# Kernel tuning notes

Measured on AMD Instinct MI355X. Metric: run time of the kernel, lower is better.

## Reference

```python
import jax, jax.numpy as jnp
import numpy as np

D_MODEL = 256
N_LAYERS = 4
D_STATE = 16
EXPAND = 2
D_CONV = 4
D_INNER = EXPAND * D_MODEL
DT_RANK = (D_MODEL + 15) // 16  # ceil(d_model/16) = 16
BATCH = 8
SEQ = 2048
EPS = 1e-5


def setup_inputs() -> dict:
    key = jax.random.key(0)
    ks = jax.random.split(key, 12)
    rn = lambda k, s, sc=0.02: jax.random.normal(k, s, dtype=jnp.float32) * sc
    A_log = jnp.log(jnp.broadcast_to(jnp.arange(1, D_STATE + 1, dtype=jnp.float32),
                                     (N_LAYERS, D_INNER, D_STATE)))
    return {
        "x": jax.random.normal(ks[0], (BATCH, SEQ, 2), dtype=jnp.float32),
        "w_in": rn(ks[1], (D_MODEL, 2), 0.5),
        "b_in": jnp.zeros((D_MODEL,), jnp.float32),
        "norm_w": jnp.ones((N_LAYERS, D_MODEL), jnp.float32),
        "in_proj_w": rn(ks[2], (N_LAYERS, 2 * D_INNER, D_MODEL)),
        "conv_w": rn(ks[3], (N_LAYERS, D_INNER, 1, D_CONV), 0.1),
        "conv_b": jnp.zeros((N_LAYERS, D_INNER), jnp.float32),
        "x_proj_w": rn(ks[4], (N_LAYERS, DT_RANK + 2 * D_STATE, D_INNER)),
        "dt_proj_w": rn(ks[5], (N_LAYERS, D_INNER, DT_RANK), 0.1),
        "dt_proj_b": rn(ks[6], (N_LAYERS, D_INNER), 0.1),
        "A_log": A_log,
        "D_skip": jnp.ones((N_LAYERS, D_INNER), jnp.float32),
        "out_proj_w": rn(ks[7], (N_LAYERS, D_MODEL, D_INNER)),
        "w_head": rn(ks[8], (1, D_MODEL), 0.1),
        "b_head": jnp.zeros((1,), jnp.float32),
    }


def _rmsnorm(x, w):
    return x * jax.lax.rsqrt(jnp.mean(x * x, axis=-1, keepdims=True) + EPS) * w


def _causal_dw_conv(x, w, b):
    # x: (B, L, C); w: (C, 1, K) depthwise; causal left-pad K-1
    xt = jnp.swapaxes(x, 1, 2)  # (B, C, L)
    y = jax.lax.conv_general_dilated(xt, w, (1,), [(D_CONV - 1, 0)],
                                     dimension_numbers=("NCH", "OIH", "NCH"),
                                     feature_group_count=D_INNER)
    return jnp.swapaxes(y + b[None, :, None], 1, 2)


def _selective_scan(u, delta, A, Bm, Cm, Dp):
    # u, delta: (B, L, E); A: (E, N); Bm, Cm: (B, L, N); Dp: (E,)
    dA = jnp.exp(delta[..., None] * A)                 # (B, L, E, N)
    dBu = (delta * u)[..., None] * Bm[:, :, None, :]   # (B, L, E, N)

    def step(h, t):
        dA_t, dBu_t = t
        h = dA_t * h + dBu_t
        return h, h

    h0 = jnp.zeros((u.shape[0], A.shape[0], A.shape[1]), u.dtype)
    _, hs = jax.lax.scan(step, h0, (jnp.swapaxes(dA, 0, 1), jnp.swapaxes(dBu, 0, 1)))
    y = jnp.einsum("lben,bln->ble", hs, Cm)            # (B, L, E)
    return y + u * Dp


def _mamba_block(x, in_w, cw, cb, xp_w, dtw, dtb, A_log, Dp, out_w):
    xz = x @ in_w.T                                    # (B, L, 2E)
    u, z = jnp.split(xz, 2, axis=-1)
    u = jax.nn.silu(_causal_dw_conv(u, cw, cb))
    dbc = u @ xp_w.T                                   # (B, L, dt_rank + 2N)
    delta = jax.nn.softplus(dbc[..., :DT_RANK] @ dtw.T + dtb)
    Bm = dbc[..., DT_RANK:DT_RANK + D_STATE]
    Cm = dbc[..., DT_RANK + D_STATE:]
    y = _selective_scan(u, delta, -jnp.exp(A_log), Bm, Cm, Dp)
    return (y * jax.nn.silu(z)) @ out_w.T


def reference(x, w_in, b_in, norm_w, in_proj_w, conv_w, conv_b, x_proj_w,
              dt_proj_w, dt_proj_b, A_log, D_skip, out_proj_w, w_head, b_head):
    h = x @ w_in.T + b_in                              # (B, L, d_model)
    for i in range(N_LAYERS):
        h = h + _mamba_block(_rmsnorm(h, norm_w[i]), in_proj_w[i], conv_w[i],
                             conv_b[i], x_proj_w[i], dt_proj_w[i], dt_proj_b[i],
                             A_log[i], D_skip[i], out_proj_w[i])
    return (h @ w_head.T + b_head)[..., 0]             # (B, L)
```

## Files before the change

kernel.cpp:

```cpp
#include <hip/hip_runtime.h>
#include <hip/hip_bf16.h>

#define BATCH 8
#define SEQ   2048
#define DM    256
#define DI    512
#define DS    16
#define DTR   16
#define NL    4
#define ROWS  (BATCH*SEQ)
#define NCH   32
#define CHL   64
#define NF    576

typedef __attribute__((ext_vector_type(8))) __bf16 bh8;
typedef __attribute__((ext_vector_type(4))) float f4;

#if __has_builtin(__builtin_amdgcn_exp2f)
#define EXP2(x) __builtin_amdgcn_exp2f(x)
#else
#define EXP2(x) exp2f(x)
#endif
#define LOG2E 1.4426950408889634f

__device__ __forceinline__ float bf2f(unsigned short u) {
    union { unsigned int i; float f; } v; v.i = ((unsigned int)u) << 16; return v.f;
}
__device__ __forceinline__ float4 us4f(ushort4 q) {
    return make_float4(bf2f(q.x), bf2f(q.y), bf2f(q.z), bf2f(q.w));
}
__device__ __forceinline__ float ldg1(const void* p, int i, int bf) {
    if (bf) return bf2f(((const unsigned short*)p)[i]);
    return ((const float*)p)[i];
}
__device__ __forceinline__ float4 ldg4(const void* p, int i, int bf) {
    if (bf) return us4f(*(const ushort4*)(((const unsigned short*)p) + i));
    return *(const float4*)(((const float*)p) + i);
}
__device__ __forceinline__ unsigned short f2bs(float f) {
    union { float f; unsigned u; } x; x.f = f;
    unsigned r = (x.u + 0x7fffu + ((x.u >> 16) & 1u)) >> 16;
    return (unsigned short)r;
}
__device__ __forceinline__ float fsilu(float x) {
    return x * __builtin_amdgcn_rcpf(1.0f + __expf(-x));
}
__device__ __forceinline__ float fsoftplus(float x) {
    return (x > 15.0f) ? x : __logf(1.0f + __expf(x));
}
__device__ __forceinline__ void pow16(float e1, float* pw) {
    float p2 = e1 * e1, p3 = p2 * e1, p4 = p2 * p2;
    float p5 = p4 * e1, p6 = p4 * p2, p7 = p4 * p3, p8 = p4 * p4;
    pw[0] = e1; pw[1] = p2; pw[2] = p3; pw[3] = p4;
    pw[4] = p5; pw[5] = p6; pw[6] = p7; pw[7] = p8;
    pw[8]  = p8 * e1; pw[9]  = p8 * p2; pw[10] = p8 * p3; pw[11] = p8 * p4;
    pw[12] = p8 * p5; pw[13] = p8 * p6; pw[14] = p8 * p7; pw[15] = p8 * p8;
}

typedef const __attribute__((address_space(1))) unsigned int* gas_t;
typedef __attribute__((address_space(3))) unsigned int* las_t;
__device__ __forceinline__ void gl16(const void* g, void* l) {
    __builtin_amdgcn_global_load_lds((gas_t)g, (las_t)l, 16, 0, 0);
}

__global__ void k_probe(const void* x, const void* A_log, int* flag) {
    int t = threadIdx.x;
    float v = bf2f(((const unsigned short*)x)[2 * t]);
    int bad = (fabsf(v) < 32.0f) ? 0 : 1;
    for (int o = 1; o < 64; o <<= 1) bad += __shfl_xor(bad, o);
    int bf = (bad > 8) ? 0 : 1;
    int nb = 0;
    for (int j = 0; j < 64; j++) {
        int e = ((j * 64 + t) * 17) & 32767;
        int n = e & 15;
        float a = ldg1(A_log, e, bf);
        float ea = __expf(a);
        if (fabsf(ea - (float)(n + 1)) > 0.02f * (float)(n + 1)) nb = 1;
    }
    for (int o = 1; o < 64; o <<= 1) nb += __shfl_xor(nb, o);
    if (t == 0) { flag[0] = bf; flag[1] = (nb == 0) ? 1 : 0; }
}

__global__ __launch_bounds__(256) void k_prep(const void* dtw, const void* xpw,
                                              const void* ipw, const void* norm_w,
                                              unsigned short* Wc, unsigned short* Wip,
                                              const int* flag) {
    int bf = *flag;
    int blk = blockIdx.x;
    int t = threadIdx.x;
    if (blk < NL * NF) {
        int l = blk / NF, r = blk % NF;
        unsigned short* out = Wc + ((size_t)l * NF + r) * DI;
#pragma unroll
        for (int p = 0; p < 2; p++) {
            int k = t + p * 256;
            float v = 0.0f;
            if (r < 512) {
                const int db = l * DI * DTR + r * DTR;
                const int xb = l * 48 * DI;
#pragma unroll
                for (int j = 0; j < 16; j++)
                    v = fmaf(ldg1(dtw, db + j, bf), ldg1(xpw, xb + j * DI + k, bf), v);
            } else if (r < 544) {
                v = ldg1(xpw, l * 48 * DI + (16 + r - 512) * DI + k, bf);
            }
            out[k] = f2bs(v);
        }
    } else {
        int b2 = blk - NL * NF;
        int l = b2 >> 10, r = b2 & 1023;
        float v = ldg1(ipw, (l * 1024 + r) * 256 + t, bf) * ldg1(norm_w, l * 256 + t, bf);
        Wip[((size_t)l * 1024 + r) * 256 + t] = f2bs(v);
    }
}

__global__ __launch_bounds__(256) void k_inproj(const void* x, const void* w_in, const void* b_in,
                                                unsigned short* h, float* rssq, const int* flag) {
    int bf = *flag;
    int row = blockIdx.x, e = threadIdx.x;
    float x0 = ldg1(x, row * 2 + 0, bf), x1 = ldg1(x, row * 2 + 1, bf);
    float w0 = ldg1(w_in, e * 2 + 0, bf), w1 = ldg1(w_in, e * 2 + 1, bf);
    float bb = ldg1(b_in, e, bf);
    unsigned short hb = f2bs(fmaf(x0, w0, fmaf(x1, w1, bb)));
    h[(size_t)row * DM + e] = hb;
    float hv = bf2f(hb);
    float ss = hv * hv;
#pragma unroll
    for (int o = 1; o < 64; o <<= 1) ss += __shfl_xor(ss, o);
    if ((e & 63) == 0) rssq[(size_t)row * 4 + (e >> 6)] = ss;
}

#define ASTR 72

__global__ __launch_bounds__(256, 4) void k_ipconv(const unsigned short* A, const unsigned short* W,
                                                   int w_off, unsigned short* xz, unsigned short* u,
                                                   const float* rssq, const void* cw, const void* cb,
                                                   int layer, const int* flag) {
    int bf = *flag;
    constexpr int K = DM;
    constexpr int TSTR = 136;
    __shared__ unsigned short SMEM[144 * TSTR];
    unsigned short* As  = SMEM;
    unsigned short* As2 = SMEM + 8192;
    unsigned short* Ws  = SMEM + 9216;

    int bm = blockIdx.x, bn = blockIdx.y;
    bool ublk = (bn < 4);
    int t = threadIdx.x;
    int w = t >> 6, lane = t & 63;
    int wm = w >> 1, wn = w & 1;
    int lr = lane & 15, quad = lane >> 4;
    int crow = lane >> 3;
    int ccol = ((lane & 7) ^ (lane >> 3)) * 8;

    f4 acc[4][4];
    f4 acc5[4];
#pragma unroll
    for (int i = 0; i < 4; i++) {
        acc5[i] = f4{0.f, 0.f, 0.f, 0.f};
#pragma unroll
        for (int j = 0; j < 4; j++) acc[i][j] = f4{0.f, 0.f, 0.f, 0.f};
    }

    for (int k0 = 0; k0 < K; k0 += 64) {
        __syncthreads();
#pragma unroll
        for (int i = 0; i < 4; i++) {
            int ci = w * 4 + i;
            int r = ci * 8 + crow;
            gl16(A + (size_t)(bm * 128 + r) * K + k0 + ccol, &As[ci * 512]);
        }
        if (ublk && w < 2) {
            int rg = bm * 128 - 16 + w * 8 + crow;
            if (rg < 0) rg = 0;
            gl16(A + (size_t)rg * K + k0 + ccol, &As2[w * 512]);
        }
#pragma unroll
        for (int i = 0; i < 4; i++) {
            int ci = w * 4 + i;
            int r = ci * 8 + crow;
            gl16(W + (size_t)w_off + (size_t)(bn * 128 + r) * K + k0 + ccol, &Ws[ci * 512]);
        }
        __syncthreads();
#pragma unroll
        for (int ks = 0; ks < 64; ks += 32) {
            int csw = (ks + quad * 8) ^ ((lr & 7) << 3);
            bh8 af[4];
#pragma unroll
            for (int i = 0; i < 4; i++)
                af[i] = *(const bh8*)&As[(wm * 64 + i * 16 + lr) * 64 + csw];
            bh8 wf[4];
#pragma unroll
            for (int j = 0; j < 4; j++)
                wf[j] = *(const bh8*)&Ws[(wn * 64 + j * 16 + lr) * 64 + csw];
#pragma unroll
            for (int i = 0; i < 4; i++)
#pragma unroll
                for (int j = 0; j < 4; j++)
                    acc[i][j] = __builtin_amdgcn_mfma_f32_16x16x32_bf16(af[i], wf[j], acc[i][j], 0, 0, 0);
            if (ublk && wm == 0) {
                bh8 a5 = *(const bh8*)&As2[lr * 64 + csw];
#pragma unroll
                for (int j = 0; j < 4; j++)
                    acc5[j] = __builtin_amdgcn_mfma_f32_16x16x32_bf16(a5, wf[j], acc5[j], 0, 0, 0);
            }
        }
    }
    __syncthreads();
    unsigned short* Tile = SMEM;
#pragma unroll
    for (int i = 0; i < 4; i++) {
        int rl = wm * 64 + i * 16 + quad * 4;
        float sc4[4];
#pragma unroll
        for (int r = 0; r < 4; r++) {
            float4 q4 = *(const float4*)&rssq[(size_t)(bm * 128 + rl + r) * 4];
            sc4[r] = rsqrtf((q4.x + q4.y + q4.z + q4.w) * (1.0f / (float)DM) + 1e-5f);
        }
#pragma unroll
        for (int j = 0; j < 4; j++) {
            int cl = wn * 64 + j * 16 + lr;
#pragma unroll
            for (int r = 0; r < 4; r++)
                Tile[(rl + r) * TSTR + cl] = f2bs(acc[i][j][r] * sc4[r]);
        }
    }
    if (ublk && wm == 0) {
#pragma unroll
        for (int r = 0; r < 4; r++) {
            int er = quad * 4 + r;
            int rg = bm * 128 - 16 + er;
            if (rg < 0) rg = 0;
            float4 q4 = *(const float4*)&rssq[(size_t)rg * 4];
            float sc = rsqrtf((q4.x + q4.y + q4.z + q4.w) * (1.0f / (float)DM) + 1e-5f);
#pragma unroll
            for (int j = 0; j < 4; j++) {
                int cl = wn * 64 + j * 16 + lr;
                Tile[(128 + er) * TSTR + cl] = f2bs(acc5[j][r] * sc);
            }
        }
    }
    __syncthreads();
    if (!ublk) {
#pragma unroll
        for (int i = 0; i < 8; i++) {
            int ch = t + i * 256;
            int r = ch >> 4, qc = (ch & 15) * 8;
            uint4 v = *(uint4*)&Tile[r * TSTR + qc];
            *(uint4*)&xz[(size_t)(bm * 128 + r) * 1024 + bn * 128 + qc] = v;
        }
    } else {
        int col4 = t & 31, rowg = t >> 5;
        int c0 = col4 * 4;
        int dg = bn * 128 + c0;
        float4 wv0 = ldg4(cw, (layer * DI + dg + 0) * 4, bf);
        float4 wv1 = ldg4(cw, (layer * DI + dg + 1) * 4, bf);
        float4 wv2 = ldg4(cw, (layer * DI + dg + 2) * 4, bf);
        float4 wv3 = ldg4(cw, (layer * DI + dg + 3) * 4, bf);
        float4 bb = ldg4(cb, layer * DI + dg, bf);
        bool bstart = ((bm & 15) == 0);
        int r0 = rowg * 16;
        auto ldrow = [&](int q) -> float4 {
            if (q < 0) {
                if (bstart) return make_float4(0.f, 0.f, 0.f, 0.f);
                return us4f(*(const ushort4*)&Tile[(144 + q) * TSTR + c0]);
            }
            return us4f(*(const ushort4*)&Tile[q * TSTR + c0]);
        };
        float4 xm3 = ldrow(r0 - 3), xm2 = ldrow(r0 - 2), xm1 = ldrow(r0 - 1);
        for (int rr = r0; rr < r0 + 16; rr++) {
            float4 x0 = us4f(*(const ushort4*)&Tile[rr * TSTR + c0]);
            float a0 = bb.x; a0 = fmaf(wv0.x, xm3.x, a0); a0 = fmaf(wv0.y, xm2.x, a0); a0 = fmaf(wv0.z, xm1.x, a0); a0 = fmaf(wv0.w, x0.x, a0);
            float a1 = bb.y; a1 = fmaf(wv1.x, xm3.y, a1); a1 = fmaf(wv1.y, xm2.y, a1); a1 = fmaf(wv1.z, xm1.y, a1); a1 = fmaf(wv1.w, x0.y, a1);
            float a2 = bb.z; a2 = fmaf(wv2.x, xm3.z, a2); a2 = fmaf(wv2.y, xm2.z, a2); a2 = fmaf(wv2.z, xm1.z, a2); a2 = fmaf(wv2.w, x0.z, a2);
            float a3 = bb.w; a3 = fmaf(wv3.x, xm3.w, a3); a3 = fmaf(wv3.y, xm2.w, a3); a3 = fmaf(wv3.z, xm1.w, a3); a3 = fmaf(wv3.w, x0.w, a3);
            ushort4 o = { f2bs(fsilu(a0)), f2bs(fsilu(a1)), f2bs(fsilu(a2)), f2bs(fsilu(a3)) };
            *(ushort4*)&u[(size_t)(bm * 128 + rr) * DI + dg] = o;
            xm3 = xm2; xm2 = xm1; xm1 = x0;
        }
    }
}

template <int BN, bool ADD, bool SCALE, bool RSUM, bool WINT>
__global__ __launch_bounds__(256, 4) void k_mfma(const unsigned short* A, const void* W, int w_off,
                                                 unsigned short* Cp, float* rssq,
                                                 int N, int K, const int* flag) {
    int bf = *flag;
    __shared__ unsigned short SMEM[(128 + BN) * ASTR];
    unsigned short* As = SMEM;
    unsigned short* Ws = SMEM + 128 * 64;
    constexpr int NT = BN / 32;
    constexpr int TSTR = BN + 8;

    int bm = blockIdx.x, bn = blockIdx.y;
    int t = threadIdx.x;
    int w = t >> 6, lane = t & 63;
    int wm = w >> 1, wn = w & 1;
    int lr = lane & 15, quad = lane >> 4;
    int crow = lane >> 3;
    int ccol = ((lane & 7) ^ (lane >> 3)) * 8;

    f4 acc[4][NT];
#pragma unroll
    for (int i = 0; i < 4; i++)
#pragma unroll
        for (int j = 0; j < NT; j++) acc[i][j] = f4{0.f, 0.f, 0.f, 0.f};

    for (int k0 = 0; k0 < K; k0 += 64) {
        __syncthreads();
#pragma unroll
        for (int i = 0; i < 4; i++) {
            int ci = w * 4 + i;
            int r = ci * 8 + crow;
            gl16(A + (size_t)(bm * 128 + r) * K + k0 + ccol, &As[ci * 512]);
        }
        if (WINT || bf) {
#pragma unroll
            for (int i = 0; i < BN / 32; i++) {
                int ci = w * (BN / 32) + i;
                int r = ci * 8 + crow;
                gl16((const unsigned short*)W + (size_t)w_off +
                         (size_t)(bn * BN + r) * K + k0 + ccol,
                     &Ws[ci * 512]);
            }
        } else {
#pragma unroll
            for (int i = 0; i < BN * 8 / 256; i++) {
                int ch = t + i * 256;
                int r = ch >> 3, kc = (ch & 7) * 8;
                size_t off = (size_t)w_off + (size_t)(bn * BN + r) * K + k0 + kc;
                const float* src = (const float*)W + off;
                float4 a0 = *(const float4*)src;
                float4 a1 = *(const float4*)(src + 4);
                ushort4 v0 = { f2bs(a0.x), f2bs(a0.y), f2bs(a0.z), f2bs(a0.w) };
                ushort4 v1 = { f2bs(a1.x), f2bs(a1.y), f2bs(a1.z), f2bs(a1.w) };
                unsigned short* dst = &Ws[r * 64 + (kc ^ ((r & 7) << 3))];
                *(ushort4*)dst = v0;
                *(ushort4*)(dst + 4) = v1;
            }
        }
        __syncthreads();
#pragma unroll
        for (int ks = 0; ks < 64; ks += 32) {
            int csw = (ks + quad * 8) ^ ((lr & 7) << 3);
            bh8 af[4];
#pragma unroll
            for (int i = 0; i < 4; i++)
                af[i] = *(const bh8*)&As[(wm * 64 + i * 16 + lr) * 64 + csw];
            bh8 wf[NT];
#pragma unroll
            for (int j = 0; j < NT; j++)
                wf[j] = *(const bh8*)&Ws[(wn * (BN / 2) + j * 16 + lr) * 64 + csw];
#pragma unroll
            for (int i = 0; i < 4; i++)
#pragma unroll
                for (int j = 0; j < NT; j++)
                    acc[i][j] = __builtin_amdgcn_mfma_f32_16x16x32_bf16(af[i], wf[j], acc[i][j], 0, 0, 0);
        }
    }
    __syncthreads();
    unsigned short* Tile = SMEM;
#pragma unroll
    for (int i = 0; i < 4; i++) {
        int rl = wm * 64 + i * 16 + quad * 4;
        float sc4[4];
        if (SCALE) {
#pragma unroll
            for (int r = 0; r < 4; r++) {
                float4 q4 = *(const float4*)&rssq[(size_t)(bm * 128 + rl + r) * 4];
                sc4[r] = rsqrtf((q4.x + q4.y + q4.z + q4.w) * (1.0f / (float)DM) + 1e-5f);
            }
        }
#pragma unroll
        for (int j = 0; j < NT; j++) {
            int cl = wn * (BN / 2) + j * 16 + lr;
#pragma unroll
            for (int r = 0; r < 4; r++) {
                float vv = acc[i][j][r];
                if (SCALE) vv *= sc4[r];
                Tile[(rl + r) * TSTR + cl] = f2bs(vv);
            }
        }
    }
    __syncthreads();
    constexpr int CPT = 128 * BN / 8 / 256;
#pragma unroll
    for (int i = 0; i < CPT; i++) {
        int ch = t + i * 256;
        int r = ch / (BN / 8), qc = (ch % (BN / 8)) * 8;
        uint4 v = *(uint4*)&Tile[r * TSTR + qc];
        size_t gidx = (size_t)(bm * 128 + r) * N + bn * BN + qc;
        if (ADD) {
            uint4 c = *(uint4*)&Cp[gidx];
            unsigned short* vp = (unsigned short*)&v;
            unsigned short* cp2 = (unsigned short*)&c;
            uint4 ov;
            unsigned short* op = (unsigned short*)&ov;
            float ssq = 0.0f;
#pragma unroll
            for (int e = 0; e < 8; e++) {
                op[e] = f2bs(bf2f(vp[e]) + bf2f(cp2[e]));
                if (RSUM) { float hv = bf2f(op[e]); ssq = fmaf(hv, hv, ssq); }
            }
            *(uint4*)&Cp[gidx] = ov;
            if (RSUM) {
#pragma unroll
                for (int o2 = 1; o2 < 8; o2 <<= 1) ssq += __shfl_xor(ssq, o2);
                if ((lane & 7) == 0) rssq[(size_t)(bm * 128 + r) * 4 + bn] = ssq;
            }
        } else {
            *(uint4*)&Cp[gidx] = v;
        }
    }
}

__global__ __launch_bounds__(256, 4) void k_fused(const unsigned short* A, const unsigned short* Wc,
                                                  int w_off, unsigned short* delta, float* BC,
                                                  const void* dtb, int layer, const int* flag) {
    int bf = *flag;
    __shared__ unsigned short SMEM[(128 + 64) * ASTR];
    unsigned short* As = SMEM;
    unsigned short* Ws = SMEM + 128 * 64;
    constexpr int TSTR = 72;

    int bm = blockIdx.x, bn = blockIdx.y;
    int t = threadIdx.x;
    int w = t >> 6, lane = t & 63;
    int wm = w >> 1, wn = w & 1;
    int lr = lane & 15, quad = lane >> 4;
    int crow = lane >> 3;
    int ccol = ((lane & 7) ^ (lane >> 3)) * 8;

    f4 acc[4][2];
#pragma unroll
    for (int i = 0; i < 4; i++)
#pragma unroll
        for (int j = 0; j < 2; j++) acc[i][j] = f4{0.f, 0.f, 0.f, 0.f};

    for (int k0 = 0; k0 < DI; k0 += 64) {
        __syncthreads();
#pragma unroll
        for (int i = 0; i < 4; i++) {
            int ci = w * 4 + i;
            int r = ci * 8 + crow;
            gl16(A + (size_t)(bm * 128 + r) * DI + k0 + ccol, &As[ci * 512]);
        }
#pragma unroll
        for (int i = 0; i < 2; i++) {
            int ci = w * 2 + i;
            int r = ci * 8 + crow;
            gl16(Wc + (size_t)w_off + (size_t)(bn * 64 + r) * DI + k0 + ccol, &Ws[ci * 512]);
        }
        __syncthreads();
#pragma unroll
        for (int ks = 0; ks < 64; ks += 32) {
            int csw = (ks + quad * 8) ^ ((lr & 7) << 3);
            bh8 af[4];
#pragma unroll
            for (int i = 0; i < 4; i++)
                af[i] = *(const bh8*)&As[(wm * 64 + i * 16 + lr) * 64 + csw];
            bh8 wf[2];
#pragma unroll
            for (int j = 0; j < 2; j++)
                wf[j] = *(const bh8*)&Ws[(wn * 32 + j * 16 + lr) * 64 + csw];
#pragma unroll
            for (int i = 0; i < 4; i++)
#pragma unroll
                for (int j = 0; j < 2; j++)
                    acc[i][j] = __builtin_amdgcn_mfma_f32_16x16x32_bf16(af[i], wf[j], acc[i][j], 0, 0, 0);
        }
    }
    if (bn < 8) {
        __syncthreads();
        unsigned short* Tile = SMEM;
#pragma unroll
        for (int i = 0; i < 4; i++) {
            int rl = wm * 64 + i * 16 + quad * 4;
#pragma unroll
            for (int j = 0; j < 2; j++) {
                int cl = wn * 32 + j * 16 + lr;
                float bb = ldg1(dtb, layer * DI + bn * 64 + cl, bf);
#pragma unroll
                for (int r = 0; r < 4; r++)
                    Tile[(rl + r) * TSTR + cl] = f2bs(fsoftplus(acc[i][j][r] + bb));
            }
        }
        __syncthreads();
#pragma unroll
        for (int i = 0; i < 4; i++) {
            int ch = t + i * 256;
            int r = ch >> 3, qc = (ch & 7) * 8;
            uint4 v = *(uint4*)&Tile[r * TSTR + qc];
            *(uint4*)&delta[(size_t)(bm * 128 + r) * DI + bn * 64 + qc] = v;
        }
    } else {
#pragma unroll
        for (int i = 0; i < 4; i++) {
            int row0 = bm * 128 + wm * 64 + i * 16 + quad * 4;
#pragma unroll
            for (int j = 0; j < 2; j++) {
                int col = bn * 64 + wn * 32 + j * 16 + lr;
                if (col < 544) {
#pragma unroll
                    for (int r = 0; r < 4; r++)
                        BC[(size_t)(row0 + r) * 32 + (col - 512)] = acc[i][j][r];
                }
            }
        }
    }
}

__global__ __launch_bounds__(256) void k_scan1(const unsigned short* delta, const unsigned short* u,
                                               const float* BC, const void* A_log, float* Sb, float* E,
                                               int layer, const int* flag) {
    int bf = flag[0], sA = flag[1];
    int x = blockIdx.x;
    int dg = x & 1, c = (x >> 1) & (NCH - 1), b = x >> 6;
    int tid = threadIdx.x;
    int d = dg * 256 + tid;
    int t0 = c * CHL;

    __shared__ float sB[CHL][16];
    {
        int r = tid >> 2, q = tid & 3;
        *(float4*)&sB[r][q * 4] =
            *(const float4*)(BC + ((size_t)b * SEQ + t0 + r) * 32 + q * 4);
    }

    float A2[16];
#pragma unroll
    for (int n4 = 0; n4 < 4; n4++) {
        float4 a4 = ldg4(A_log, (layer * DI + d) * DS + n4 * 4, bf);
        A2[n4 * 4 + 0] = -__expf(a4.x) * LOG2E;
        A2[n4 * 4 + 1] = -__expf(a4.y) * LOG2E;
        A2[n4 * 4 + 2] = -__expf(a4.z) * LOG2E;
        A2[n4 * 4 + 3] = -__expf(a4.w) * LOG2E;
    }
    float h[16];
#pragma unroll
    for (int n = 0; n < 16; n++) h[n] = 0.0f;
    float S = 0.0f;

    const unsigned short* dp = delta + ((size_t)b * SEQ + t0) * DI + d;
    const unsigned short* up = u + ((size_t)b * SEQ + t0) * DI + d;

    float dl0[4], uu0[4];
#pragma unroll
    for (int j = 0; j < 4; j++) { dl0[j] = bf2f(dp[j * DI]); uu0[j] = bf2f(up[j * DI]); }
    __syncthreads();

    for (int s = 0; s < CHL / 4; s++) {
        int sn = (s + 1 < CHL / 4) ? (s + 1) : s;
        float dl1[4], uu1[4];
#pragma unroll
        for (int j = 0; j < 4; j++) {
            dl1[j] = bf2f(dp[(sn * 4 + j) * DI]);
            uu1[j] = bf2f(up[(sn * 4 + j) * DI]);
        }
#pragma unroll
        for (int j = 0; j < 4; j++) {
            int t = s * 4 + j;
            float dlt = dl0[j], uu = uu0[j];
            float du = dlt * uu;
            S += dlt;
            if (sA) {
                float pw[16];
                pow16(EXP2(-dlt * LOG2E), pw);
#pragma unroll
                for (int n4 = 0; n4 < 4; n4++) {
                    float4 Bv = *(const float4*)&sB[t][n4 * 4];
                    int n = n4 * 4;
                    h[n + 0] = fmaf(pw[n + 0], h[n + 0], du * Bv.x);
                    h[n + 1] = fmaf(pw[n + 1], h[n + 1], du * Bv.y);
                    h[n + 2] = fmaf(pw[n + 2], h[n + 2], du * Bv.z);
                    h[n + 3] = fmaf(pw[n + 3], h[n + 3], du * Bv.w);
                }
            } else {
#pragma unroll
                for (int n4 = 0; n4 < 4; n4++) {
                    float4 Bv = *(const float4*)&sB[t][n4 * 4];
                    int n = n4 * 4;
                    float a0 = EXP2(dlt * A2[n + 0]); h[n + 0] = fmaf(a0, h[n + 0], du * Bv.x);
                    float a1 = EXP2(dlt * A2[n + 1]); h[n + 1] = fmaf(a1, h[n + 1], du * Bv.y);
                    float a2 = EXP2(dlt * A2[n + 2]); h[n + 2] = fmaf(a2, h[n + 2], du * Bv.z);
                    float a3 = EXP2(dlt * A2[n + 3]); h[n + 3] = fmaf(a3, h[n + 3], du * Bv.w);
                }
            }
        }
#pragma unroll
        for (int j = 0; j < 4; j++) { dl0[j] = dl1[j]; uu0[j] = uu1[j]; }
    }
    Sb[((size_t)b * NCH + c) * DI + d] = S;
    float* Ed = E + (((size_t)b * NCH + c) * DI + d) * DS;
#pragma unroll
    for (int n4 = 0; n4 < 4; n4++)
        *(float4*)(Ed + n4 * 4) = make_float4(h[n4 * 4], h[n4 * 4 + 1], h[n4 * 4 + 2], h[n4 * 4 + 3]);
}

__global__ __launch_bounds__(256) void k_stitch(const float* Sb, const void* A_log, float* E,
                                                int layer, const int* flag) {
    int bf = flag[0];
    int g = blockIdx.x * 256 + threadIdx.x;
    int b = g >> 13, r = g & 8191;
    int d = r >> 4;
    float A2a = -__expf(ldg1(A_log, (layer * DI + d) * DS + (r & 15), bf)) * LOG2E;
    size_t ebase = (size_t)b * NCH * (DI * DS) + r;
    float H = 0.0f;
    for (int c = 0; c < NCH; c++) {
        float p = EXP2(A2a * Sb[((size_t)b * NCH + c) * DI + d]);
        size_t idx = ebase + (size_t)c * (DI * DS);
        float e = E[idx];
        E[idx] = H;
        H = fmaf(p, H, e);
    }
}

__global__ __launch_bounds__(256) void k_scan2(const unsigned short* delta, const unsigned short* u,
                                               const float* BC, const void* A_log, const void* D_skip,
                                               const unsigned short* xz, const float* E,
                                               unsigned short* g, int layer, const int* flag) {
    int bf = flag[0], sA = flag[1];
    int x = blockIdx.x;
    int dg = x & 1, c = (x >> 1) & (NCH - 1), b = x >> 6;
    int tid = threadIdx.x;
    int d = dg * 256 + tid;
    int t0 = c * CHL;

    __shared__ float sBC[CHL][32];
#pragma unroll
    for (int k2 = 0; k2 < 2; k2++) {
        int fi = k2 * 256 + tid;
        int r = fi >> 3, q = fi & 7;
        *(float4*)&sBC[r][q * 4] =
            *(const float4*)(BC + ((size_t)b * SEQ + t0 + r) * 32 + q * 4);
    }

    float A2[16];
#pragma unroll
    for (int n4 = 0; n4 < 4; n4++) {
        float4 a4 = ldg4(A_log, (layer * DI + d) * DS + n4 * 4, bf);
        A2[n4 * 4 + 0] = -__expf(a4.x) * LOG2E;
        A2[n4 * 4 + 1] = -__expf(a4.y) * LOG2E;
        A2[n4 * 4 + 2] = -__expf(a4.z) * LOG2E;
        A2[n4 * 4 + 3] = -__expf(a4.w) * LOG2E;
    }
    float Dp = ldg1(D_skip, layer * DI + d, bf);

    float h[16];
    const float* E0 = E + (((size_t)b * NCH + c) * DI + d) * DS;
#pragma unroll
    for (int n4 = 0; n4 < 4; n4++) {
        float4 h4 = *(const float4*)(E0 + n4 * 4);
        h[n4 * 4 + 0] = h4.x; h[n4 * 4 + 1] = h4.y; h[n4 * 4 + 2] = h4.z; h[n4 * 4 + 3] = h4.w;
    }

    const unsigned short* dp = delta + ((size_t)b * SEQ + t0) * DI + d;
    const unsigned short* up = u + ((size_t)b * SEQ + t0) * DI + d;
    const unsigned short* zp = xz + ((size_t)b * SEQ + t0) * (2 * DI) + DI + d;
    unsigned short* gp = g + ((size_t)b * SEQ + t0) * DI + d;

    float dl0[4], uu0[4], zz0[4];
#pragma unroll
    for (int j = 0; j < 4; j++) {
        dl0[j] = bf2f(dp[j * DI]); uu0[j] = bf2f(up[j * DI]); zz0[j] = bf2f(zp[j * (2 * DI)]);
    }
    __syncthreads();

    for (int s = 0; s < CHL / 4; s++) {
        int sn = (s + 1 < CHL / 4) ? (s + 1) : s;
        float dl1[4], uu1[4], zz1[4];
#pragma unroll
        for (int j = 0; j < 4; j++) {
            dl1[j] = bf2f(dp[(sn * 4 + j) * DI]);
            uu1[j] = bf2f(up[(sn * 4 + j) * DI]);
            zz1[j] = bf2f(zp[(sn * 4 + j) * (2 * DI)]);
        }
#pragma unroll
        for (int j = 0; j < 4; j++) {
            int t = s * 4 + j;
            float dlt = dl0[j], uu = uu0[j], zz = zz0[j];
            float du = dlt * uu;
            float y = 0.0f;
            if (sA) {
                float pw[16];
                pow16(EXP2(-dlt * LOG2E), pw);
#pragma unroll
                for (int n4 = 0; n4 < 4; n4++) {
                    float4 Bv = *(const float4*)&sBC[t][n4 * 4];
                    float4 Cv = *(const float4*)&sBC[t][16 + n4 * 4];
                    int n = n4 * 4;
                    h[n + 0] = fmaf(pw[n + 0], h[n + 0], du * Bv.x); y = fmaf(Cv.x, h[n + 0], y);
                    h[n + 1] = fmaf(pw[n + 1], h[n + 1], du * Bv.y); y = fmaf(Cv.y, h[n + 1], y);
                    h[n + 2] = fmaf(pw[n + 2], h[n + 2], du * Bv.z); y = fmaf(Cv.z, h[n + 2], y);
                    h[n + 3] = fmaf(pw[n + 3], h[n + 3], du * Bv.w); y = fmaf(Cv.w, h[n + 3], y);
                }
            } else {
#pragma unroll
                for (int n4 = 0; n4 < 4; n4++) {
                    float4 Bv = *(const float4*)&sBC[t][n4 * 4];
                    float4 Cv = *(const float4*)&sBC[t][16 + n4 * 4];
                    int n = n4 * 4;
                    float a0 = EXP2(dlt * A2[n + 0]); h[n + 0] = fmaf(a0, h[n + 0], du * Bv.x); y = fmaf(Cv.x, h[n + 0], y);
                    float a1 = EXP2(dlt * A2[n + 1]); h[n + 1] = fmaf(a1, h[n + 1], du * Bv.y); y = fmaf(Cv.y, h[n + 1], y);
                    float a2 = EXP2(dlt * A2[n + 2]); h[n + 2] = fmaf(a2, h[n + 2], du * Bv.z); y = fmaf(Cv.z, h[n + 2], y);
                    float a3 = EXP2(dlt * A2[n + 3]); h[n + 3] = fmaf(a3, h[n + 3], du * Bv.w); y = fmaf(Cv.w, h[n + 3], y);
                }
            }
            float yt = fmaf(uu, Dp, y);
            gp[(size_t)t * DI] = f2bs(yt * fsilu(zz));
        }
#pragma unroll
        for (int j = 0; j < 4; j++) { dl0[j] = dl1[j]; uu0[j] = uu1[j]; zz0[j] = zz1[j]; }
    }
}

__global__ __launch_bounds__(256) void k_head(const unsigned short* h, const void* w_head,
                                              const void* b_head, void* out, const int* flag) {
    int bf = *flag;
    int wv = threadIdx.x >> 6, ln = threadIdx.x & 63;
    int row = blockIdx.x * 4 + wv;
    float4 v = us4f(*(const ushort4*)(h + (size_t)row * DM + ln * 4));
    float4 w = ldg4(w_head, ln * 4, bf);
    float s = v.x * w.x + v.y * w.y + v.z * w.z + v.w * w.w;
    for (int o = 1; o < 64; o <<= 1) s += __shfl_xor(s, o);
    if (ln == 0) {
        s += ldg1(b_head, 0, bf);
        if (bf) ((__hip_bfloat16*)out)[row] = __float2bfloat16(s);
        else    ((float*)out)[row] = s;
    }
}

extern "C" void kernel_launch(void* const* d_in, const int* in_sizes, int n_in,
                              void* d_out, int out_size, void* d_ws, size_t ws_size,
                              hipStream_t stream) {
    (void)in_sizes; (void)n_in; (void)out_size; (void)ws_size;
    const void* x      = d_in[0];
    const void* w_in   = d_in[1];
    const void* b_in   = d_in[2];
    const void* norm_w = d_in[3];
    const void* ipw    = d_in[4];
    const void* cw     = d_in[5];
    const void* cb     = d_in[6];
    const void* xpw    = d_in[7];
    const void* dtw    = d_in[8];
    const void* dtb    = d_in[9];
    const void* A_log  = d_in[10];
    const void* D_skip = d_in[11];
    const void* opw    = d_in[12];
    const void* w_head = d_in[13];
    const void* b_head = d_in[14];

    float* ws    = (float*)d_ws;
    unsigned short* h     = (unsigned short*)ws;
    float*          rssq  = ws + 4194304;
    float*          Sb    = ws + 4194304;
    float*          E     = ws + 4718592;
    unsigned short* xz    = (unsigned short*)(ws + 8388608);
    unsigned short* u     = (unsigned short*)(ws + 25165824);
    float*          BC    = ws + 33554432;
    unsigned short* delta = (unsigned short*)(ws + 34340864);
    unsigned short* Wcomb = (unsigned short*)(ws + 38535168);
    unsigned short* Wipc  = (unsigned short*)(ws + 39124992);
    int*            flag  = (int*)(ws + 42729472);

    k_probe<<<1, 64, 0, stream>>>(x, A_log, flag);
    k_prep<<<NL * NF + NL * 1024, 256, 0, stream>>>(dtw, xpw, ipw, norm_w, Wcomb, Wipc, flag);
    k_inproj<<<ROWS, 256, 0, stream>>>(x, w_in, b_in, h, rssq, flag);

    for (int layer = 0; layer < NL; layer++) {
        k_ipconv<<<dim3(ROWS / 128, 8), 256, 0, stream>>>(
            h, Wipc, layer * 2 * DI * DM, xz, u, rssq, cw, cb, layer, flag);
        k_fused<<<dim3(ROWS / 128, NF / 64), 256, 0, stream>>>(
            u, Wcomb, layer * NF * DI, delta, BC, dtb, layer, flag);
        k_scan1<<<BATCH * NCH * 2, 256, 0, stream>>>(delta, u, BC, A_log, Sb, E, layer, flag);
        k_stitch<<<BATCH * DI * DS / 256, 256, 0, stream>>>(Sb, A_log, E, layer, flag);
        k_scan2<<<BATCH * NCH * 2, 256, 0, stream>>>(delta, u, BC, A_log, D_skip, xz, E,
                                                     u , layer, flag);
        k_mfma<64, true, false, true, false><<<dim3(ROWS / 128, DM / 64), 256, 0, stream>>>(
            u, opw, layer * DM * DI, h, rssq, DM, DI, flag);
    }

    k_head<<<ROWS / 4, 256, 0, stream>>>(h, w_head, b_head, d_out, flag);
}
```

Measured before the change: 578.4 us.

## Split scan state dimension across two half-waves to double scan parallelism

The chunked scan kernels now assign each channel to two lanes, each holding 8 of the 16 state elements, and launch twice as many blocks. The partial C·h outputs are combined with a cross-half-wave shuffle, and only one lane writes each output. This is meant to raise occupancy and latency hiding in the scan, which previously had only 512 blocks with 16-element register state per thread. The cost is that both lanes redundantly load delta, u and z, compute pow16 or exp, and pay an extra shuffle per timestep, and the global loads are less coalesced (32 channels per wave instead of 64).

```diff
diff --git a/kernel.cpp b/kernel.cpp
--- a/kernel.cpp
+++ b/kernel.cpp
@@ -515,9 +515,11 @@
                                                int layer, const int* flag) {
     int bf = flag[0], sA = flag[1];
     int x = blockIdx.x;
-    int dg = x & 1, c = (x >> 1) & (NCH - 1), b = x >> 6;
+    int dg = x & 3, c = (x >> 2) & (NCH - 1), b = x >> 7;
     int tid = threadIdx.x;
-    int d = dg * 256 + tid;
+    int wv = tid >> 6, lane = tid & 63;
+    int ch = lane & 31, sh = lane >> 5;
+    int d = dg * 128 + wv * 32 + ch;
     int t0 = c * CHL;
 
     __shared__ float sB[CHL][16];
@@ -527,18 +529,18 @@
             *(const float4*)(BC + ((size_t)b * SEQ + t0 + r) * 32 + q * 4);
     }
 
-    float A2[16];
-#pragma unroll
-    for (int n4 = 0; n4 < 4; n4++) {
-        float4 a4 = ldg4(A_log, (layer * DI + d) * DS + n4 * 4, bf);
+    float A2[8];
+#pragma unroll
+    for (int n4 = 0; n4 < 2; n4++) {
+        float4 a4 = ldg4(A_log, (layer * DI + d) * DS + sh * 8 + n4 * 4, bf);
         A2[n4 * 4 + 0] = -__expf(a4.x) * LOG2E;
         A2[n4 * 4 + 1] = -__expf(a4.y) * LOG2E;
         A2[n4 * 4 + 2] = -__expf(a4.z) * LOG2E;
         A2[n4 * 4 + 3] = -__expf(a4.w) * LOG2E;
     }
-    float h[16];
-#pragma unroll
-    for (int n = 0; n < 16; n++) h[n] = 0.0f;
+    float h[8];
+#pragma unroll
+    for (int n = 0; n < 8; n++) h[n] = 0.0f;
     float S = 0.0f;
 
     const unsigned short* dp = delta + ((size_t)b * SEQ + t0) * DI + d;
@@ -567,18 +569,18 @@
                 float pw[16];
                 pow16(EXP2(-dlt * LOG2E), pw);
 #pragma unroll
-                for (int n4 = 0; n4 < 4; n4++) {
-                    float4 Bv = *(const float4*)&sB[t][n4 * 4];
+                for (int n4 = 0; n4 < 2; n4++) {
+                    float4 Bv = *(const float4*)&sB[t][sh * 8 + n4 * 4];
                     int n = n4 * 4;
-                    h[n + 0] = fmaf(pw[n + 0], h[n + 0], du * Bv.x);
-                    h[n + 1] = fmaf(pw[n + 1], h[n + 1], du * Bv.y);
-                    h[n + 2] = fmaf(pw[n + 2], h[n + 2], du * Bv.z);
-                    h[n + 3] = fmaf(pw[n + 3], h[n + 3], du * Bv.w);
+                    h[n + 0] = fmaf(pw[sh * 8 + n + 0], h[n + 0], du * Bv.x);
+                    h[n + 1] = fmaf(pw[sh * 8 + n + 1], h[n + 1], du * Bv.y);
+                    h[n + 2] = fmaf(pw[sh * 8 + n + 2], h[n + 2], du * Bv.z);
+                    h[n + 3] = fmaf(pw[sh * 8 + n + 3], h[n + 3], du * Bv.w);
                 }
             } else {
 #pragma unroll
-                for (int n4 = 0; n4 < 4; n4++) {
-                    float4 Bv = *(const float4*)&sB[t][n4 * 4];
+                for (int n4 = 0; n4 < 2; n4++) {
+                    float4 Bv = *(const float4*)&sB[t][sh * 8 + n4 * 4];
                     int n = n4 * 4;
                     float a0 = EXP2(dlt * A2[n + 0]); h[n + 0] = fmaf(a0, h[n + 0], du * Bv.x);
                     float a1 = EXP2(dlt * A2[n + 1]); h[n + 1] = fmaf(a1, h[n + 1], du * Bv.y);
@@ -590,10 +592,10 @@
 #pragma unroll
         for (int j = 0; j < 4; j++) { dl0[j] = dl1[j]; uu0[j] = uu1[j]; }
     }
-    Sb[((size_t)b * NCH + c) * DI + d] = S;
-    float* Ed = E + (((size_t)b * NCH + c) * DI + d) * DS;
-#pragma unroll
-    for (int n4 = 0; n4 < 4; n4++)
+    if (sh == 0) Sb[((size_t)b * NCH + c) * DI + d] = S;
+    float* Ed = E + (((size_t)b * NCH + c) * DI + d) * DS + sh * 8;
+#pragma unroll
+    for (int n4 = 0; n4 < 2; n4++)
         *(float4*)(Ed + n4 * 4) = make_float4(h[n4 * 4], h[n4 * 4 + 1], h[n4 * 4 + 2], h[n4 * 4 + 3]);
 }
 
@@ -621,9 +623,11 @@
                                                unsigned short* g, int layer, const int* flag) {
     int bf = flag[0], sA = flag[1];
     int x = blockIdx.x;
-    int dg = x & 1, c = (x >> 1) & (NCH - 1), b = x >> 6;
+    int dg = x & 3, c = (x >> 2) & (NCH - 1), b = x >> 7;
     int tid = threadIdx.x;
-    int d = dg * 256 + tid;
+    int wv = tid >> 6, lane = tid & 63;
+    int ch = lane & 31, sh = lane >> 5;
+    int d = dg * 128 + wv * 32 + ch;
     int t0 = c * CHL;
 
     __shared__ float sBC[CHL][32];
@@ -635,10 +639,10 @@
             *(const float4*)(BC + ((size_t)b * SEQ + t0 + r) * 32 + q * 4);
     }
 
-    float A2[16];
-#pragma unroll
-    for (int n4 = 0; n4 < 4; n4++) {
-        float4 a4 = ldg4(A_log, (layer * DI + d) * DS + n4 * 4, bf);
+    float A2[8];
+#pragma unroll
+    for (int n4 = 0; n4 < 2; n4++) {
+        float4 a4 = ldg4(A_log, (layer * DI + d) * DS + sh * 8 + n4 * 4, bf);
         A2[n4 * 4 + 0] = -__expf(a4.x) * LOG2E;
         A2[n4 * 4 + 1] = -__expf(a4.y) * LOG2E;
         A2[n4 * 4 + 2] = -__expf(a4.z) * LOG2E;
@@ -646,10 +650,10 @@
     }
     float Dp = ldg1(D_skip, layer * DI + d, bf);
 
-    float h[16];
-    const float* E0 = E + (((size_t)b * NCH + c) * DI + d) * DS;
-#pragma unroll
-    for (int n4 = 0; n4 < 4; n4++) {
+    float h[8];
+    const float* E0 = E + (((size_t)b * NCH + c) * DI + d) * DS + sh * 8;
+#pragma unroll
+    for (int n4 = 0; n4 < 2; n4++) {
         float4 h4 = *(const float4*)(E0 + n4 * 4);
         h[n4 * 4 + 0] = h4.x; h[n4 * 4 + 1] = h4.y; h[n4 * 4 + 2] = h4.z; h[n4 * 4 + 3] = h4.w;
     }
@@ -685,20 +689,20 @@
                 float pw[16];
                 pow16(EXP2(-dlt * LOG2E), pw);
 #pragma unroll
-                for (int n4 = 0; n4 < 4; n4++) {
-                    float4 Bv = *(const float4*)&sBC[t][n4 * 4];
-                    float4 Cv = *(const float4*)&sBC[t][16 + n4 * 4];
+                for (int n4 = 0; n4 < 2; n4++) {
+                    float4 Bv = *(const float4*)&sBC[t][sh * 8 + n4 * 4];
+                    float4 Cv = *(const float4*)&sBC[t][16 + sh * 8 + n4 * 4];
                     int n = n4 * 4;
-                    h[n + 0] = fmaf(pw[n + 0], h[n + 0], du * Bv.x); y = fmaf(Cv.x, h[n + 0], y);
-                    h[n + 1] = fmaf(pw[n + 1], h[n + 1], du * Bv.y); y = fmaf(Cv.y, h[n + 1], y);
-                    h[n + 2] = fmaf(pw[n + 2], h[n + 2], du * Bv.z); y = fmaf(Cv.z, h[n + 2], y);
-                    h[n + 3] = fmaf(pw[n + 3], h[n + 3], du * Bv.w); y = fmaf(Cv.w, h[n + 3], y);
+                    h[n + 0] = fmaf(pw[sh * 8 + n + 0], h[n + 0], du * Bv.x); y = fmaf(Cv.x, h[n + 0], y);
+                    h[n + 1] = fmaf(pw[sh * 8 + n + 1], h[n + 1], du * Bv.y); y = fmaf(Cv.y, h[n + 1], y);
+                    h[n + 2] = fmaf(pw[sh * 8 + n + 2], h[n + 2], du * Bv.z); y = fmaf(Cv.z, h[n + 2], y);
+                    h[n + 3] = fmaf(pw[sh * 8 + n + 3], h[n + 3], du * Bv.w); y = fmaf(Cv.w, h[n + 3], y);
                 }
             } else {
 #pragma unroll
-                for (int n4 = 0; n4 < 4; n4++) {
-                    float4 Bv = *(const float4*)&sBC[t][n4 * 4];
-                    float4 Cv = *(const float4*)&sBC[t][16 + n4 * 4];
+                for (int n4 = 0; n4 < 2; n4++) {
+                    float4 Bv = *(const float4*)&sBC[t][sh * 8 + n4 * 4];
+                    float4 Cv = *(const float4*)&sBC[t][16 + sh * 8 + n4 * 4];
                     int n = n4 * 4;
                     float a0 = EXP2(dlt * A2[n + 0]); h[n + 0] = fmaf(a0, h[n + 0], du * Bv.x); y = fmaf(Cv.x, h[n + 0], y);
                     float a1 = EXP2(dlt * A2[n + 1]); h[n + 1] = fmaf(a1, h[n + 1], du * Bv.y); y = fmaf(Cv.y, h[n + 1], y);
@@ -706,8 +710,11 @@
                     float a3 = EXP2(dlt * A2[n + 3]); h[n + 3] = fmaf(a3, h[n + 3], du * Bv.w); y = fmaf(Cv.w, h[n + 3], y);
                 }
             }
-            float yt = fmaf(uu, Dp, y);
-            gp[(size_t)t * DI] = f2bs(yt * fsilu(zz));
+            y += __shfl_xor(y, 32);
+            if (sh == 0) {
+                float yt = fmaf(uu, Dp, y);
+                gp[(size_t)t * DI] = f2bs(yt * fsilu(zz));
+            }
         }
 #pragma unroll
         for (int j = 0; j < 4; j++) { dl0[j] = dl1[j]; uu0[j] = uu1[j]; zz0[j] = zz1[j]; }
@@ -772,9 +779,9 @@
             h, Wipc, layer * 2 * DI * DM, xz, u, rssq, cw, cb, layer, flag);
         k_fused<<<dim3(ROWS / 128, NF / 64), 256, 0, stream>>>(
             u, Wcomb, layer * NF * DI, delta, BC, dtb, layer, flag);
-        k_scan1<<<BATCH * NCH * 2, 256, 0, stream>>>(delta, u, BC, A_log, Sb, E, layer, flag);
+        k_scan1<<<BATCH * NCH * 4, 256, 0, stream>>>(delta, u, BC, A_log, Sb, E, layer, flag);
         k_stitch<<<BATCH * DI * DS / 256, 256, 0, stream>>>(Sb, A_log, E, layer, flag);
-        k_scan2<<<BATCH * NCH * 2, 256, 0, stream>>>(delta, u, BC, A_log, D_skip, xz, E,
+        k_scan2<<<BATCH * NCH * 4, 256, 0, stream>>>(delta, u, BC, A_log, D_skip, xz, E,
                                                      u , layer, flag);
         k_mfma<64, true, false, true, false><<<dim3(ROWS / 128, DM / 64), 256, 0, stream>>>(
             u, opw, layer * DM * DI, h, rssq, DM, DI, flag);
```

Result: slower. 1.566 ms (+170.7%).
